# Kernel optimization log

Measured on AMD Instinct MI355X. Metric: run time of the kernel, lower is better.

## Reference

```python
import jax, jax.numpy as jnp
import numpy as np

B = 2097152  # batch
H = 2        # GRU hidden size


def _gru_cell(x, h, w_ih, w_hh, b_ih, b_hh):
    # torch.nn.GRUCell math. w_ih: [3H, I], w_hh: [3H, H]
    gi = x @ w_ih.T + b_ih  # [B, 3H]
    gh = h @ w_hh.T + b_hh  # [B, 3H]
    i_r, i_z, i_n = jnp.split(gi, 3, axis=-1)
    h_r, h_z, h_n = jnp.split(gh, 3, axis=-1)
    r = jax.nn.sigmoid(i_r + h_r)
    z = jax.nn.sigmoid(i_z + h_z)
    n = jnp.tanh(i_n + r * h_n)
    return (1.0 - z) * n + z * h


def setup_inputs() -> dict:
    key = jax.random.key(0)
    ks = jax.random.split(key, 14)
    f32 = jnp.float32
    inp = {
        "x": jax.random.normal(ks[0], (B, 18), dtype=f32),
        # r_up: GRUCell(2, 2)
        "w_ih_up": 0.3 * jax.random.normal(ks[1], (3 * H, 2), dtype=f32),
        "w_hh_up": 0.3 * jax.random.normal(ks[2], (3 * H, H), dtype=f32),
        "b_ih_up": 0.1 * jax.random.normal(ks[3], (3 * H,), dtype=f32),
        "b_hh_up": 0.1 * jax.random.normal(ks[4], (3 * H,), dtype=f32),
        # fc_obs: Linear(6, 2)
        "w_obs": 0.3 * jax.random.normal(ks[5], (2, 6), dtype=f32),
        "b_obs": 0.1 * jax.random.normal(ks[6], (2,), dtype=f32),
        # r_down: GRUCell(2, 2)
        "w_ih_dn": 0.3 * jax.random.normal(ks[7], (3 * H, 2), dtype=f32),
        "w_hh_dn": 0.3 * jax.random.normal(ks[8], (3 * H, H), dtype=f32),
        "b_ih_dn": 0.1 * jax.random.normal(ks[9], (3 * H,), dtype=f32),
        "b_hh_dn": 0.1 * jax.random.normal(ks[10], (3 * H,), dtype=f32),
        # fc_out: Linear(2, 1)
        "w_out": 0.3 * jax.random.normal(ks[11], (1, H), dtype=f32),
        "b_out": 0.1 * jax.random.normal(ks[12], (1,), dtype=f32),
    }
    return inp


def reference(x, w_ih_up, w_hh_up, b_ih_up, b_hh_up, w_obs, b_obs,
              w_ih_dn, w_hh_dn, b_ih_dn, b_hh_dn, w_out, b_out):
    obs = x[:, :4]            # [B, 4]
    j = x[:, 4:11]            # [B, 7]
    jd = x[:, 11:]            # [B, 7]
    jcat = jnp.stack([j, jd], axis=1)  # [B, 2, 7]

    # upward recurrence over the 7 joints, reversed order
    h = jnp.zeros((x.shape[0], H), dtype=x.dtype)
    h_up = []
    for i in reversed(range(7)):
        h = _gru_cell(jcat[:, :, i], h, w_ih_up, w_hh_up, b_ih_up, b_hh_up)
        h_up.append(h)

    # fuse observation into the hidden state
    h = jnp.concatenate([obs, h], axis=1) @ w_obs.T + b_obs  # [B, 2]

    # downward recurrence, emitting one action per joint
    acts = []
    for i in range(7):
        h = _gru_cell(h_up[i], h, w_ih_dn, w_hh_dn, b_ih_dn, b_hh_dn)
        acts.append(h @ w_out.T + b_out)  # [B, 1]
    return jnp.concatenate(acts, axis=1)  # [B, 7]
```

## Files before the change

kernel.cpp:

```cpp
#include <hip/hip_runtime.h>


using v2f = __attribute__((ext_vector_type(2))) float;

__device__ __forceinline__ float fexp2(float x) { return __builtin_amdgcn_exp2f(x); }
__device__ __forceinline__ float frcp(float x)  { return __builtin_amdgcn_rcpf(x); }

struct Cell {
    v2f wr0, wr1, ur0, ur1, br;
    v2f wz0, wz1, uz0, uz1, bz;
    v2f wn0, wn1, bni;
    v2f un0, un1, bnh;
};

__global__ void prep_kernel(
    const float* __restrict__ w_ih_up, const float* __restrict__ w_hh_up,
    const float* __restrict__ b_ih_up, const float* __restrict__ b_hh_up,
    const float* __restrict__ w_obs,   const float* __restrict__ b_obs,
    const float* __restrict__ w_ih_dn, const float* __restrict__ w_hh_dn,
    const float* __restrict__ b_ih_dn, const float* __restrict__ b_hh_dn,
    const float* __restrict__ w_out,   const float* __restrict__ b_out,
    float* __restrict__ ws)
{
    if (threadIdx.x != 0 || blockIdx.x != 0) return;
    const float s1 = -1.4426950408889634f;
    const float s2 =  2.8853900817779268f;
    #pragma unroll
    for (int c = 0; c < 2; ++c) {
        const float* wi = c ? w_ih_dn : w_ih_up;
        const float* wh = c ? w_hh_dn : w_hh_up;
        const float* bi = c ? b_ih_dn : b_ih_up;
        const float* bh = c ? b_hh_dn : b_hh_up;
        float* o = ws + c * 64;
        o[0] = s1*wi[0]; o[1] = s1*wi[2];  o[2] = s1*wi[1]; o[3] = s1*wi[3];
        o[4] = s1*wh[0]; o[5] = s1*wh[2];  o[6] = s1*wh[1]; o[7] = s1*wh[3];
        o[8] = s1*(bi[0]+bh[0]); o[9] = s1*(bi[1]+bh[1]);
        o[10] = s1*wi[4]; o[11] = s1*wi[6]; o[12] = s1*wi[5]; o[13] = s1*wi[7];
        o[14] = s1*wh[4]; o[15] = s1*wh[6]; o[16] = s1*wh[5]; o[17] = s1*wh[7];
        o[18] = s1*(bi[2]+bh[2]); o[19] = s1*(bi[3]+bh[3]);
        o[20] = s2*wi[8]; o[21] = s2*wi[10]; o[22] = s2*wi[9]; o[23] = s2*wi[11];
        o[24] = s2*bi[4]; o[25] = s2*bi[5];
        o[26] = s2*wh[8]; o[27] = s2*wh[10]; o[28] = s2*wh[9]; o[29] = s2*wh[11];
        o[30] = s2*bh[4]; o[31] = s2*bh[5];
    }
    #pragma unroll
    for (int i = 0; i < 12; ++i) ws[128 + i] = w_obs[i];
    ws[140] = b_obs[0]; ws[141] = b_obs[1];
    ws[142] = w_out[0]; ws[143] = w_out[1];
    ws[144] = b_out[0];
}

__device__ __forceinline__ void gru(const Cell& c, float x0, float x1, v2f& h) {
    v2f gr = c.br + c.wr0 * x0 + c.wr1 * x1 + c.ur0 * h.x + c.ur1 * h.y;
    v2f gz = c.bz + c.wz0 * x0 + c.wz1 * x1 + c.uz0 * h.x + c.uz1 * h.y;
    v2f r  = (v2f){ frcp(1.0f + fexp2(gr.x)), frcp(1.0f + fexp2(gr.y)) };
    v2f z  = (v2f){ frcp(1.0f + fexp2(gz.x)), frcp(1.0f + fexp2(gz.y)) };
    v2f in = c.bni + c.wn0 * x0 + c.wn1 * x1;
    v2f hn = c.bnh + c.un0 * h.x + c.un1 * h.y;
    v2f a  = in + r * hn;
    v2f n  = (v2f){ 1.0f - 2.0f * frcp(1.0f + fexp2(a.x)),
                    1.0f - 2.0f * frcp(1.0f + fexp2(a.y)) };
    h = n + z * (h - n);
}

__global__ __launch_bounds__(256) void recpolicy_kernel(
    const float* __restrict__ x, const float* __restrict__ W,
    float* __restrict__ out, int n)
{
    __shared__ float lds[4608];
    const int tid  = threadIdx.x;
    const int row0 = blockIdx.x * 256;
    const int rows = min(256, n - row0);

    if (rows == 256) {
        const float4* src = reinterpret_cast<const float4*>(x + (size_t)row0 * 18);
        float4* dst = reinterpret_cast<float4*>(lds);
        #pragma unroll
        for (int i = 0; i < 5; ++i) {
            int idx = tid + i * 256;
            if (idx < 1152) dst[idx] = src[idx];
        }
    } else {
        for (int idx = tid; idx < rows * 18; idx += 256)
            lds[idx] = x[(size_t)row0 * 18 + idx];
    }

    const Cell up = *reinterpret_cast<const Cell*>(W);
    const Cell dn = *reinterpret_cast<const Cell*>(W + 64);

    __syncthreads();

    float xv[18];
    {
        const float2* r2 = reinterpret_cast<const float2*>(lds + tid * 18);
        #pragma unroll
        for (int i = 0; i < 9; ++i) { float2 v = r2[i]; xv[2*i] = v.x; xv[2*i+1] = v.y; }
    }
    __syncthreads();

    v2f h = (v2f){0.0f, 0.0f};
    v2f hu[7];
    #pragma unroll
    for (int k = 0; k < 7; ++k) {
        const int i = 6 - k;
        gru(up, xv[4 + i], xv[11 + i], h);
        hu[k] = h;
    }

    {
        v2f t = (v2f){W[140], W[141]};
        #pragma unroll
        for (int c = 0; c < 4; ++c)
            t += (v2f){W[128 + c], W[134 + c]} * xv[c];
        t += (v2f){W[132], W[138]} * h.x;
        t += (v2f){W[133], W[139]} * h.y;
        h = t;
    }

    const float wo0 = W[142], wo1 = W[143], bo = W[144];
    #pragma unroll
    for (int k = 0; k < 7; ++k) {
        gru(dn, hu[k].x, hu[k].y, h);
        lds[tid * 7 + k] = fmaf(wo0, h.x, fmaf(wo1, h.y, bo));
    }
    __syncthreads();

    if (rows == 256) {
        float4* dst = reinterpret_cast<float4*>(out + (size_t)row0 * 7);
        const float4* src = reinterpret_cast<const float4*>(lds);
        #pragma unroll
        for (int i = 0; i < 2; ++i) {
            int idx = tid + i * 256;
            if (idx < 448) dst[idx] = src[idx];
        }
    } else {
        for (int idx = tid; idx < rows * 7; idx += 256)
            out[(size_t)row0 * 7 + idx] = lds[idx];
    }
}

extern "C" void kernel_launch(void* const* d_in, const int* in_sizes, int n_in,
                              void* d_out, int out_size, void* d_ws, size_t ws_size,
                              hipStream_t stream) {
    const float* x       = (const float*)d_in[0];
    const float* w_ih_up = (const float*)d_in[1];
    const float* w_hh_up = (const float*)d_in[2];
    const float* b_ih_up = (const float*)d_in[3];
    const float* b_hh_up = (const float*)d_in[4];
    const float* w_obs   = (const float*)d_in[5];
    const float* b_obs   = (const float*)d_in[6];
    const float* w_ih_dn = (const float*)d_in[7];
    const float* w_hh_dn = (const float*)d_in[8];
    const float* b_ih_dn = (const float*)d_in[9];
    const float* b_hh_dn = (const float*)d_in[10];
    const float* w_out   = (const float*)d_in[11];
    const float* b_out   = (const float*)d_in[12];
    float* out = (float*)d_out;
    float* ws  = (float*)d_ws;

    prep_kernel<<<1, 64, 0, stream>>>(
        w_ih_up, w_hh_up, b_ih_up, b_hh_up, w_obs, b_obs,
        w_ih_dn, w_hh_dn, b_ih_dn, b_hh_dn, w_out, b_out, ws);

    const int n = in_sizes[0] / 18;
    const int block = 256;
    const int grid = (n + block - 1) / block;
    recpolicy_kernel<<<grid, block, 0, stream>>>(x, ws, out, n);
}
```

Baseline: 54.75 us.

## Use persistent blocks with register-prefetch of next input tile

Switches the kernel to a grid-stride persistent loop capped at 2048 blocks. Each block prefetches the next 256-row tile into registers while computing the current one, and uses separate LDS buffers for input and output. The goal is to overlap global load latency with GRU compute and to cut block launch overhead. Rows that do not fill a full 256-row tile are no longer handled, and more registers and LDS per block may lower occupancy.

Result: no change. 54.03 us (-1.3%).

```diff
diff --git a/kernel.cpp b/kernel.cpp
--- a/kernel.cpp
+++ b/kernel.cpp
@@ -67,75 +67,82 @@
     const float* __restrict__ x, const float* __restrict__ W,
     float* __restrict__ out, int n)
 {
-    __shared__ float lds[4608];
-    const int tid  = threadIdx.x;
-    const int row0 = blockIdx.x * 256;
-    const int rows = min(256, n - row0);
-
-    if (rows == 256) {
-        const float4* src = reinterpret_cast<const float4*>(x + (size_t)row0 * 18);
-        float4* dst = reinterpret_cast<float4*>(lds);
-        #pragma unroll
-        for (int i = 0; i < 5; ++i) {
-            int idx = tid + i * 256;
-            if (idx < 1152) dst[idx] = src[idx];
-        }
-    } else {
-        for (int idx = tid; idx < rows * 18; idx += 256)
-            lds[idx] = x[(size_t)row0 * 18 + idx];
-    }
+    __shared__ float sin_[4608];
+    __shared__ float sout[1792];
+    const int tid = threadIdx.x;
+    const int NT = n >> 8;
+    const int stride = gridDim.x;
 
     const Cell up = *reinterpret_cast<const Cell*>(W);
     const Cell dn = *reinterpret_cast<const Cell*>(W + 64);
 
-    __syncthreads();
+    int t = blockIdx.x;
+    if (t >= NT) return;
 
-    float xv[18];
+    const float4* xs = reinterpret_cast<const float4*>(x);
+    float4 nx0, nx1, nx2, nx3, nx4;
     {
-        const float2* r2 = reinterpret_cast<const float2*>(lds + tid * 18);
-        #pragma unroll
-        for (int i = 0; i < 9; ++i) { float2 v = r2[i]; xv[2*i] = v.x; xv[2*i+1] = v.y; }
-    }
-    __syncthreads();
-
-    v2f h = (v2f){0.0f, 0.0f};
-    v2f hu[7];
-    #pragma unroll
-    for (int k = 0; k < 7; ++k) {
-        const int i = 6 - k;
-        gru(up, xv[4 + i], xv[11 + i], h);
-        hu[k] = h;
+        size_t b = (size_t)t * 1152;
+        nx0 = xs[b + tid];       nx1 = xs[b + 256 + tid];
+        nx2 = xs[b + 512 + tid]; nx3 = xs[b + 768 + tid];
+        if (tid < 128) nx4 = xs[b + 1024 + tid];
     }
 
-    {
-        v2f t = (v2f){W[140], W[141]};
+    while (true) {
+        {
+            float4* d = reinterpret_cast<float4*>(sin_);
+            d[tid] = nx0; d[256 + tid] = nx1;
+            d[512 + tid] = nx2; d[768 + tid] = nx3;
+            if (tid < 128) d[1024 + tid] = nx4;
+        }
+        __syncthreads();
+
+        const int tn = t + stride;
+        if (tn < NT) {
+            size_t b = (size_t)tn * 1152;
+            nx0 = xs[b + tid];       nx1 = xs[b + 256 + tid];
+            nx2 = xs[b + 512 + tid]; nx3 = xs[b + 768 + tid];
+            if (tid < 128) nx4 = xs[b + 1024 + tid];
+        }
+
+        const float* row = sin_ + tid * 18;
+
+        v2f h = (v2f){0.0f, 0.0f};
+        v2f hu[7];
         #pragma unroll
-        for (int c = 0; c < 4; ++c)
-            t += (v2f){W[128 + c], W[134 + c]} * xv[c];
-        t += (v2f){W[132], W[138]} * h.x;
-        t += (v2f){W[133], W[139]} * h.y;
-        h = t;
-    }
+        for (int k = 0; k < 7; ++k) {
+            const int i = 6 - k;
+            gru(up, row[4 + i], row[11 + i], h);
+            hu[k] = h;
+        }
 
-    const float wo0 = W[142], wo1 = W[143], bo = W[144];
-    #pragma unroll
-    for (int k = 0; k < 7; ++k) {
-        gru(dn, hu[k].x, hu[k].y, h);
-        lds[tid * 7 + k] = fmaf(wo0, h.x, fmaf(wo1, h.y, bo));
-    }
-    __syncthreads();
+        {
+            v2f acc = (v2f){W[140], W[141]};
+            #pragma unroll
+            for (int c = 0; c < 4; ++c)
+                acc += (v2f){W[128 + c], W[134 + c]} * row[c];
+            acc += (v2f){W[132], W[138]} * h.x;
+            acc += (v2f){W[133], W[139]} * h.y;
+            h = acc;
+        }
 
-    if (rows == 256) {
-        float4* dst = reinterpret_cast<float4*>(out + (size_t)row0 * 7);
-        const float4* src = reinterpret_cast<const float4*>(lds);
+        const float wo0 = W[142], wo1 = W[143], bo = W[144];
         #pragma unroll
-        for (int i = 0; i < 2; ++i) {
-            int idx = tid + i * 256;
-            if (idx < 448) dst[idx] = src[idx];
+        for (int k = 0; k < 7; ++k) {
+            gru(dn, hu[k].x, hu[k].y, h);
+            sout[tid * 7 + k] = fmaf(wo0, h.x, fmaf(wo1, h.y, bo));
         }
-    } else {
-        for (int idx = tid; idx < rows * 7; idx += 256)
-            out[(size_t)row0 * 7 + idx] = lds[idx];
+        __syncthreads();
+
+        {
+            const float4* so = reinterpret_cast<const float4*>(sout);
+            float4* dst = reinterpret_cast<float4*>(out + (size_t)t * 1792);
+            dst[tid] = so[tid];
+            if (tid < 192) dst[256 + tid] = so[256 + tid];
+        }
+
+        if (tn >= NT) break;
+        t = tn;
     }
 }
 
@@ -163,7 +170,7 @@
         w_ih_dn, w_hh_dn, b_ih_dn, b_hh_dn, w_out, b_out, ws);
 
     const int n = in_sizes[0] / 18;
-    const int block = 256;
-    const int grid = (n + block - 1) / block;
-    recpolicy_kernel<<<grid, block, 0, stream>>>(x, ws, out, n);
+    const int NT = n >> 8;
+    const int grid = NT < 2048 ? NT : 2048;
+    recpolicy_kernel<<<grid, 256, 0, stream>>>(x, ws, out, n);
 }
```
